# Optimization experiments

Measured on AMD Instinct MI355X. Metric: run time of the kernel, lower is better.

The kernel has to match this reference:

```python
import jax, jax.numpy as jnp
import numpy as np

B, NPG, DEG, D, H, K, NHID, CB = 64, 512, 16, 128, 4, 5, 50, 512
N = B * NPG
E = N * DEG
TAU = 1.0
EPS = 1e-6
BN_SCALE = 1.0 / np.sqrt(1.0 + 1e-5)  # eval-mode BatchNorm, running mean=0 var=1


def _forward(x, edge_index, batch, emb, gin_W1, gin_b1, gin_W2, gin_b2, bn_gamma, bn_beta, part_W1, part_b1, part_W2, part_b2, Wq, Wk, Wv, Wo, gate_W1, gate_b1, gate_W2, gate_b2, codebook, cls_W1, cls_b1, cls_W2, cls_b2, cls_W3, cls_b3):
    # --- GIN stack: h_i <- MLP((1+eps)*h_i + sum_{j->i} h_j), eps=0 ---
    h = emb[x]  # [N, D]
    src, dst = edge_index[0], edge_index[1]
    n_layers = gin_W1.shape[0]
    for l in range(n_layers):
        agg = jax.ops.segment_sum(h[src], dst, num_segments=N)  # scatter-add neighbor messages
        z = h + agg
        z = jax.nn.relu(z @ gin_W1[l] + gin_b1[l]) @ gin_W2[l] + gin_b2[l]
        z = z * (BN_SCALE * bn_gamma[l]) + bn_beta[l]  # eval BN
        h = jax.nn.relu(z) if l < n_layers - 1 else z
    # --- to_dense_batch (equal-size graphs) + soft partitioner ---
    dense = h.reshape(B, NPG, D)
    cl = jax.nn.relu(dense @ part_W1 + part_b1) @ part_W2 + part_b2  # [B,NPG,K]
    S = jax.nn.softmax(cl / TAU, axis=-1)  # soft node->cluster assignment
    cf = jnp.einsum('bnk,bnd->bkd', S, dense) / (S.sum(1)[..., None] + EPS)
    # --- VQ codebook (l2 nearest neighbor, straight-through) ---
    flat = cf.reshape(-1, D)
    d2 = (flat * flat).sum(-1, keepdims=True) - 2.0 * flat @ codebook.T + (codebook * codebook).sum(-1)
    idx = jnp.argmin(d2, axis=-1)
    zq = cf + jax.lax.stop_gradient(codebook[idx].reshape(B, K, D) - cf)
    # --- scatter-mean graph pooling over batch vector ---
    residue = jax.ops.segment_sum(h, batch, num_segments=B) / NPG  # [B,D]
    # --- global cluster attention (4 heads), residue query vs cluster keys ---
    dh = D // H
    q = (residue @ Wq).reshape(B, H, dh)
    k = (zq @ Wk).reshape(B, K, H, dh)
    v = (zq @ Wv).reshape(B, K, H, dh)
    aw = jax.nn.softmax(jnp.einsum('bhd,bkhd->bhk', q, k) / np.sqrt(dh), axis=-1)
    att = jnp.einsum('bhk,bkhd->bhd', aw, v).reshape(B, D) @ Wo
    # --- feature-wise gated fusion ---
    cat = jnp.concatenate([residue, att], axis=-1)
    g = jax.nn.sigmoid(jax.nn.relu(cat @ gate_W1 + gate_b1) @ gate_W2 + gate_b2)
    fused = g * residue + (1.0 - g) * att
    # --- classifier MLP ---
    z1 = jax.nn.relu(fused @ cls_W1 + cls_b1)
    z2 = jax.nn.relu(z1 @ cls_W2 + cls_b2)
    return z2 @ cls_W3 + cls_b3


def setup_inputs():
    key = jax.random.key(0)
    ks = jax.random.split(key, 20)
    def lin(k, i, o):
        return jax.random.normal(k, (i, o), jnp.float32) / np.sqrt(i)
    x = jax.random.randint(ks[0], (N,), 0, 21, dtype=jnp.int32)
    srcn = jnp.repeat(jnp.arange(N, dtype=jnp.int32), DEG)
    dstn = (srcn // NPG) * NPG + jax.random.randint(ks[1], (E,), 0, NPG, dtype=jnp.int32)
    edge_index = jnp.stack([srcn, dstn])
    batch = jnp.repeat(jnp.arange(B, dtype=jnp.int32), NPG)
    return {
        'x': x, 'edge_index': edge_index, 'batch': batch,
        'emb': jax.random.normal(ks[2], (21, D), jnp.float32) * 0.02,
        'gin_W1': jax.random.normal(ks[3], (3, D, 2 * D), jnp.float32) / np.sqrt(D),
        'gin_b1': jnp.zeros((3, 2 * D), jnp.float32),
        'gin_W2': jax.random.normal(ks[4], (3, 2 * D, D), jnp.float32) / np.sqrt(2 * D),
        'gin_b2': jnp.zeros((3, D), jnp.float32),
        'bn_gamma': jnp.ones((3, D), jnp.float32),
        'bn_beta': jnp.zeros((3, D), jnp.float32),
        'part_W1': lin(ks[5], D, NHID), 'part_b1': jnp.zeros((NHID,), jnp.float32),
        'part_W2': lin(ks[6], NHID, K), 'part_b2': jnp.zeros((K,), jnp.float32),
        'Wq': lin(ks[7], D, D), 'Wk': lin(ks[8], D, D), 'Wv': lin(ks[9], D, D), 'Wo': lin(ks[10], D, D),
        'gate_W1': lin(ks[11], 2 * D, D // 2), 'gate_b1': jnp.zeros((D // 2,), jnp.float32),
        'gate_W2': lin(ks[12], D // 2, D), 'gate_b2': jnp.zeros((D,), jnp.float32),
        'codebook': jax.random.normal(ks[13], (CB, D), jnp.float32) * 0.1,
        'cls_W1': lin(ks[14], D, 4 * D), 'cls_b1': jnp.zeros((4 * D,), jnp.float32),
        'cls_W2': lin(ks[15], 4 * D, 2 * D), 'cls_b2': jnp.zeros((2 * D,), jnp.float32),
        'cls_W3': lin(ks[16], 2 * D, 2), 'cls_b3': jnp.zeros((2,), jnp.float32),
    }


def reference(x, edge_index, batch, emb, gin_W1, gin_b1, gin_W2, gin_b2, bn_gamma, bn_beta, part_W1, part_b1, part_W2, part_b2, Wq, Wk, Wv, Wo, gate_W1, gate_b1, gate_W2, gate_b2, codebook, cls_W1, cls_b1, cls_W2, cls_b2, cls_W3, cls_b3):
    return _forward(x, edge_index, batch, emb, gin_W1, gin_b1, gin_W2, gin_b2, bn_gamma, bn_beta, part_W1, part_b1, part_W2, part_b2, Wq, Wk, Wv, Wo, gate_W1, gate_b1, gate_W2, gate_b2, codebook, cls_W1, cls_b1, cls_W2, cls_b2, cls_W3, cls_b3)
```

## Files before the change

### kernel.cpp

```cpp
#include <hip/hip_runtime.h>

constexpr int B_    = 64;
constexpr int NPG_  = 512;
constexpr int D_    = 128;
constexpr int K_    = 5;
constexpr int NHID_ = 50;
constexpr int CB_   = 512;
constexpr int N_    = B_ * NPG_;
constexpr int E_    = N_ * 16;
constexpr float BN_SCALE_ = 0.99999500003749969f;
constexpr float EPS_ = 1e-6f;

typedef __attribute__((ext_vector_type(8))) short bf16x8_t;
typedef __attribute__((ext_vector_type(4))) float f32x4_t;

__device__ __forceinline__ unsigned short f2bf(float x) {
    unsigned int u = __float_as_uint(x);
    unsigned int r = (u + 0x7FFFu + ((u >> 16) & 1u)) >> 16;
    return (unsigned short)r;
}
__device__ __forceinline__ float bf2f(unsigned short b) {
    return __uint_as_float(((unsigned int)b) << 16);
}

__device__ __forceinline__ f32x4_t mfma3(bf16x8_t a0, bf16x8_t a1,
                                         bf16x8_t b0, bf16x8_t b1, f32x4_t acc) {
    acc = __builtin_amdgcn_mfma_f32_16x16x32_bf16(a1, b0, acc, 0, 0, 0);
    acc = __builtin_amdgcn_mfma_f32_16x16x32_bf16(a0, b1, acc, 0, 0, 0);
    acc = __builtin_amdgcn_mfma_f32_16x16x32_bf16(a0, b0, acc, 0, 0, 0);
    return acc;
}

__global__ void k_prep(const float* __restrict__ gw1, const float* __restrict__ gw2,
                       unsigned short* __restrict__ w1h, unsigned short* __restrict__ w1l,
                       unsigned short* __restrict__ w2h, unsigned short* __restrict__ w2l) {
    int e = blockIdx.x * 256 + threadIdx.x;
    int layer = e >> 16, rem = e & 65535;
    if (rem < 32768) {
        int k = rem >> 8, n = rem & 255;
        float v = gw1[layer * 32768 + rem];
        unsigned short h0 = f2bf(v);
        int o = layer * 32768 +
                ((((n >> 4) * 4 + (k >> 5)) * 64 + ((k >> 3) & 3) * 16 + (n & 15)) << 3) + (k & 7);
        w1h[o] = h0; w1l[o] = f2bf(v - bf2f(h0));
    } else {
        int rr = rem - 32768;
        int c = rr >> 7, n = rr & 127;
        float v = gw2[layer * 32768 + rr];
        unsigned short h0 = f2bf(v);
        int o = layer * 32768 +
                ((((n >> 4) * 8 + (c >> 5)) * 64 + ((c >> 3) & 3) * 16 + (n & 15)) << 3) + (c & 7);
        w2h[o] = h0; w2l[o] = f2bf(v - bf2f(h0));
    }
}

__global__ __launch_bounds__(512) void k_csr(const int* __restrict__ dst,
                                             int* __restrict__ rowptr,
                                             int* __restrict__ col) {
    __shared__ int cnt[512];
    __shared__ int sc[512];
    __shared__ short dstS[8192];
    int g = blockIdx.x, t = threadIdx.x;
    int base = g * 8192;
    cnt[t] = 0;
    __syncthreads();
    for (int i = t; i < 8192; i += 512) {
        int d = dst[base + i] & 511;
        dstS[i] = (short)d;
        atomicAdd(&cnt[d], 1);
    }
    __syncthreads();
    int c0 = cnt[t];
    sc[t] = c0;
    __syncthreads();
    for (int off = 1; off < 512; off <<= 1) {
        int v = sc[t];
        int add = (t >= off) ? sc[t - off] : 0;
        __syncthreads();
        sc[t] = v + add;
        __syncthreads();
    }
    int excl = sc[t] - c0;
    rowptr[g * 512 + t] = base + excl;
    cnt[t] = excl;
    if (g == 0 && t == 0) rowptr[N_] = E_;
    __syncthreads();
    for (int i = t; i < 8192; i += 512) {
        int d = dstS[i];
        int p = atomicAdd(&cnt[d], 1);
        col[base + p] = g * 512 + (i >> 4);
    }
}

constexpr int LDH = 264;
constexpr int COLCAP = 1024;
template<int L0>
__global__ __launch_bounds__(512, 8) void k_gin(
    const float* __restrict__ hIn, const int* __restrict__ rowptr,
    const int* __restrict__ col,
    const int* __restrict__ xIdx, const float* __restrict__ emb,
    const unsigned short* __restrict__ w1h, const unsigned short* __restrict__ w1l,
    const unsigned short* __restrict__ w2h, const unsigned short* __restrict__ w2l,
    const float* __restrict__ b1, const float* __restrict__ b2,
    const float* __restrict__ gamma, const float* __restrict__ beta,
    int relu_out, float* __restrict__ hOut) {
    __shared__ int colS[COLCAP];
    __shared__ unsigned short bufH[32 * LDH];
    __shared__ unsigned short bufL[32 * LDH];
    __shared__ float embS[L0 ? 21 * 128 : 1];
    __shared__ int xS[L0 ? 512 : 1];
    int i = blockIdx.x;
    int xcd = i & 7;
    int slot = i >> 3;
    int g = (slot >> 4) * 8 + xcd;
    int tile = slot & 15;
    int rowBase = g * 512 + tile * 32;
    int t = threadIdx.x;
    int w = t >> 6, l = t & 63;
    int l15 = l & 15, quad = l >> 4;
    int half = l >> 5, lane4 = l & 31;

    int ebase = rowptr[rowBase];
    int ecnt  = rowptr[rowBase + 32] - ebase;
    bool inLds = (ecnt <= COLCAP);
    if (inLds)
        for (int j = t; j < ecnt; j += 512) colS[j] = col[ebase + j];
    if constexpr (L0) {
        for (int j = t; j < 21 * 128; j += 512) embS[j] = emb[j];
        if (t < 512) xS[t] = xIdx[(rowBase & ~511) + t];
    }
    __syncthreads();

    const float4* h4 = (const float4*)hIn;
    #pragma unroll
    for (int jj = 0; jj < 2; jj++) {
        int row = w * 4 + half * 2 + jj;
        int node = rowBase + row;
        int beg = rowptr[node], end = rowptr[node + 1];
        float4 a;
        if constexpr (L0)
            a = *(const float4*)&embS[xS[node & 511] * 128 + lane4 * 4];
        else
            a = h4[(size_t)node * 32 + lane4];
        int e = beg;
        if constexpr (L0) {
            for (; e < end; e++) {
                int c = (inLds ? colS[e - ebase] : col[e]) & 511;
                float4 p = *(const float4*)&embS[xS[c] * 128 + lane4 * 4];
                a.x += p.x; a.y += p.y; a.z += p.z; a.w += p.w;
            }
        } else {
            for (; e + 8 <= end; e += 8) {
                int c[8];
                #pragma unroll
                for (int u = 0; u < 8; u++)
                    c[u] = inLds ? colS[e - ebase + u] : col[e + u];
                float4 p[8];
                #pragma unroll
                for (int u = 0; u < 8; u++)
                    p[u] = h4[(size_t)c[u] * 32 + lane4];
                #pragma unroll
                for (int u = 0; u < 8; u++) {
                    a.x += p[u].x; a.y += p[u].y; a.z += p[u].z; a.w += p[u].w;
                }
            }
            for (; e < end; e++) {
                int c = inLds ? colS[e - ebase] : col[e];
                float4 p = h4[(size_t)c * 32 + lane4];
                a.x += p.x; a.y += p.y; a.z += p.z; a.w += p.w;
            }
        }
        unsigned short h0 = f2bf(a.x), h1 = f2bf(a.y), h2s = f2bf(a.z), h3 = f2bf(a.w);
        uint2 hv, lv;
        hv.x = (unsigned)h0 | ((unsigned)h1 << 16);
        hv.y = (unsigned)h2s | ((unsigned)h3 << 16);
        lv.x = (unsigned)f2bf(a.x - bf2f(h0)) | ((unsigned)f2bf(a.y - bf2f(h1)) << 16);
        lv.y = (unsigned)f2bf(a.z - bf2f(h2s)) | ((unsigned)f2bf(a.w - bf2f(h3)) << 16);
        *(uint2*)&bufH[row * LDH + lane4 * 4] = hv;
        *(uint2*)&bufL[row * LDH + lane4 * 4] = lv;
    }
    __syncthreads();

    f32x4_t acc[2][2];
    #pragma unroll
    for (int nt = 0; nt < 2; nt++) {
        float bb = b1[w * 32 + nt * 16 + l15];
        acc[0][nt] = (f32x4_t){bb, bb, bb, bb};
        acc[1][nt] = (f32x4_t){bb, bb, bb, bb};
    }
    #pragma unroll
    for (int kk = 0; kk < 4; kk++) {
        bf16x8_t ah[2], al[2];
        #pragma unroll
        for (int mt = 0; mt < 2; mt++) {
            int addr = (mt * 16 + l15) * LDH + kk * 32 + quad * 8;
            ah[mt] = *(const bf16x8_t*)&bufH[addr];
            al[mt] = *(const bf16x8_t*)&bufL[addr];
        }
        #pragma unroll
        for (int nt = 0; nt < 2; nt++) {
            int n16 = w * 2 + nt;
            int ga = (((n16 * 4 + kk) * 64 + l) << 3);
            bf16x8_t bh = *(const bf16x8_t*)&w1h[ga];
            bf16x8_t bl = *(const bf16x8_t*)&w1l[ga];
            acc[0][nt] = mfma3(ah[0], al[0], bh, bl, acc[0][nt]);
            acc[1][nt] = mfma3(ah[1], al[1], bh, bl, acc[1][nt]);
        }
    }
    __syncthreads();

    #pragma unroll
    for (int mt = 0; mt < 2; mt++)
        #pragma unroll
        for (int nt = 0; nt < 2; nt++) {
            int colL = w * 32 + nt * 16 + l15;
            #pragma unroll
            for (int r = 0; r < 4; r++) {
                int row = mt * 16 + quad * 4 + r;
                float v = fmaxf(acc[mt][nt][r], 0.f);
                unsigned short h0 = f2bf(v);
                bufH[row * LDH + colL] = h0;
                bufL[row * LDH + colL] = f2bf(v - bf2f(h0));
            }
        }
    __syncthreads();

    f32x4_t acc2[2];
    {
        float bb = b2[w * 16 + l15];
        acc2[0] = (f32x4_t){bb, bb, bb, bb};
        acc2[1] = (f32x4_t){bb, bb, bb, bb};
    }
    #pragma unroll
    for (int kkG = 0; kkG < 8; kkG++) {
        bf16x8_t ah[2], al[2];
        #pragma unroll
        for (int mt = 0; mt < 2; mt++) {
            int addr = (mt * 16 + l15) * LDH + kkG * 32 + quad * 8;
            ah[mt] = *(const bf16x8_t*)&bufH[addr];
            al[mt] = *(const bf16x8_t*)&bufL[addr];
        }
        int ga = (((w * 8 + kkG) * 64 + l) << 3);
        bf16x8_t bh = *(const bf16x8_t*)&w2h[ga];
        bf16x8_t bl = *(const bf16x8_t*)&w2l[ga];
        acc2[0] = mfma3(ah[0], al[0], bh, bl, acc2[0]);
        acc2[1] = mfma3(ah[1], al[1], bh, bl, acc2[1]);
    }
    {
        int colC = w * 16 + l15;
        float gm = BN_SCALE_ * gamma[colC];
        float be = beta[colC];
        #pragma unroll
        for (int mt = 0; mt < 2; mt++)
            #pragma unroll
            for (int r = 0; r < 4; r++) {
                int row = mt * 16 + quad * 4 + r;
                float v = fmaf(acc2[mt][r], gm, be);
                if (relu_out) v = fmaxf(v, 0.f);
                hOut[(size_t)(rowBase + row) * 128 + colC] = v;
            }
    }
}

__global__ __launch_bounds__(256) void k_partcf(
    const float* __restrict__ h,
    const float* __restrict__ W1, const float* __restrict__ b1,
    const float* __restrict__ W2, const float* __restrict__ b2,
    float* __restrict__ pacc, float* __restrict__ pss, float* __restrict__ prs) {
    __shared__ float zt[64 * 128];
    __shared__ float ht[64 * 52];
    __shared__ float lt[64 * 5];
    __shared__ float red[128 * 6];
    __shared__ float ssred[10];
    int t = threadIdx.x;
    int blk = blockIdx.x;
    int base = blk * 64;
    #pragma unroll
    for (int i = 0; i < 32; i++) { int idx = t + i * 256; zt[idx] = h[(size_t)base * D_ + idx]; }
    __syncthreads();
    int tx = t & 63, ty = t >> 6, r0 = ty * 16;
    if (tx < NHID_) {
        float acc[16];
        float bb = b1[tx];
        #pragma unroll
        for (int r = 0; r < 16; r++) acc[r] = bb;
        for (int k = 0; k < 128; k++) {
            float w = W1[k * NHID_ + tx];
            #pragma unroll
            for (int r = 0; r < 16; r++) acc[r] = fmaf(zt[(r0 + r) * 128 + k], w, acc[r]);
        }
        #pragma unroll
        for (int r = 0; r < 16; r++) ht[(r0 + r) * 52 + tx] = fmaxf(acc[r], 0.f);
    }
    __syncthreads();
    if (tx < K_) {
        float acc[16];
        float bb = b2[tx];
        #pragma unroll
        for (int r = 0; r < 16; r++) acc[r] = bb;
        for (int c = 0; c < NHID_; c++) {
            float w = W2[c * K_ + tx];
            #pragma unroll
            for (int r = 0; r < 16; r++) acc[r] = fmaf(ht[(r0 + r) * 52 + c], w, acc[r]);
        }
        #pragma unroll
        for (int r = 0; r < 16; r++) lt[(r0 + r) * 5 + tx] = acc[r];
    }
    __syncthreads();
    if (t < 64) {
        float l0 = lt[t*5], l1 = lt[t*5+1], l2 = lt[t*5+2], l3 = lt[t*5+3], l4 = lt[t*5+4];
        float m = fmaxf(fmaxf(fmaxf(l0, l1), fmaxf(l2, l3)), l4);
        float e0 = expf(l0 - m), e1 = expf(l1 - m), e2 = expf(l2 - m),
              e3 = expf(l3 - m), e4 = expf(l4 - m);
        float inv = 1.0f / (e0 + e1 + e2 + e3 + e4);
        lt[t*5]   = e0*inv; lt[t*5+1] = e1*inv; lt[t*5+2] = e2*inv;
        lt[t*5+3] = e3*inv; lt[t*5+4] = e4*inv;
    }
    __syncthreads();
    int d = t & 127, grp = t >> 7;
    float acc[5] = {0,0,0,0,0}, ssum[5] = {0,0,0,0,0}, rs = 0;
    #pragma unroll 4
    for (int i = 0; i < 32; i++) {
        int nl = grp * 32 + i;
        float hv = zt[nl * 128 + d];
        rs += hv;
        #pragma unroll
        for (int k = 0; k < 5; k++) {
            float sv = lt[nl * 5 + k];
            acc[k] = fmaf(sv, hv, acc[k]);
            ssum[k] += sv;
        }
    }
    if (grp == 1) {
        #pragma unroll
        for (int k = 0; k < 5; k++) red[d * 6 + k] = acc[k];
        red[d * 6 + 5] = rs;
    }
    if (d == 0) {
        #pragma unroll
        for (int k = 0; k < 5; k++) ssred[grp * 5 + k] = ssum[k];
    }
    __syncthreads();
    if (grp == 0) {
        #pragma unroll
        for (int k = 0; k < 5; k++) {
            acc[k] += red[d * 6 + k];
            pacc[((size_t)blk * 5 + k) * 128 + d] = acc[k];
        }
        rs += red[d * 6 + 5];
        prs[blk * 128 + d] = rs;
        if (d < 5) pss[blk * 5 + d] = ssred[d] + ssred[5 + d];
    }
}

__global__ __launch_bounds__(1024) void k_tail(
    const float* __restrict__ pacc, const float* __restrict__ pss,
    const float* __restrict__ prs, const float* __restrict__ cbk,
    const float* __restrict__ Wq, const float* __restrict__ Wk,
    const float* __restrict__ Wv, const float* __restrict__ Wo,
    const float* __restrict__ gW1, const float* __restrict__ gb1,
    const float* __restrict__ gW2, const float* __restrict__ gb2,
    const float* __restrict__ cW1, const float* __restrict__ cb1,
    const float* __restrict__ cW2, const float* __restrict__ cb2,
    const float* __restrict__ cW3, const float* __restrict__ cb3,
    float* __restrict__ out) {
    __shared__ float cfS[5 * 128];
    __shared__ float zqS[5 * 128];
    __shared__ float catS[256];
    __shared__ float qS[128];
    __shared__ float kS[5 * 128];
    __shared__ float vS[5 * 128];
    __shared__ float awS[20];
    __shared__ float att1S[128];
    __shared__ float attP[4][128];
    __shared__ float g1P[8][64];
    __shared__ float g1S[64];
    __shared__ float g2P[4][128];
    __shared__ float fusedS[128];
    __shared__ float z1P[2][512];
    __shared__ float z1S[512];
    __shared__ float z2P[4][256];
    __shared__ float bd5[5][512];
    __shared__ int   bi5[5][512];
    __shared__ int   idxS[5];
    __shared__ float red[8];

    int g = blockIdx.x, t = threadIdx.x;

    if (t < 768) {
        int c = t >> 7, d = t & 127;
        if (c == 5) {
            float rs = 0;
            #pragma unroll
            for (int ch = 0; ch < 8; ch++) rs += prs[(g * 8 + ch) * 128 + d];
            catS[d] = rs * (1.0f / 512.0f);
        } else {
            float acc = 0, ss = 0;
            #pragma unroll
            for (int ch = 0; ch < 8; ch++) {
                int blk = g * 8 + ch;
                acc += pacc[((size_t)blk * 5 + c) * 128 + d];
                ss  += pss[blk * 5 + c];
            }
            cfS[c * 128 + d] = acc / (ss + EPS_);
        }
    }
    __syncthreads();

    if (t < 512) {
        const float4* cj = (const float4*)(cbk + (size_t)t * 128);
        float d2[5] = {0, 0, 0, 0, 0};
        #pragma unroll 8
        for (int q4 = 0; q4 < 32; q4++) {
            float4 c4 = cj[q4];
            #pragma unroll
            for (int k = 0; k < 5; k++) {
                float4 f4 = ((const float4*)(cfS + k * 128))[q4];
                float dx = f4.x - c4.x, dy = f4.y - c4.y;
                float dz = f4.z - c4.z, dw = f4.w - c4.w;
                d2[k] = fmaf(dx, dx, d2[k]); d2[k] = fmaf(dy, dy, d2[k]);
                d2[k] = fmaf(dz, dz, d2[k]); d2[k] = fmaf(dw, dw, d2[k]);
            }
        }
        #pragma unroll
        for (int k = 0; k < 5; k++) { bd5[k][t] = d2[k]; bi5[k][t] = t; }
    }
    __syncthreads();
    for (int s = 256; s > 0; s >>= 1) {
        if (t < s) {
            #pragma unroll
            for (int k = 0; k < 5; k++) {
                float bo = bd5[k][t + s]; int io = bi5[k][t + s];
                if (bo < bd5[k][t] || (bo == bd5[k][t] && io < bi5[k][t])) {
                    bd5[k][t] = bo; bi5[k][t] = io;
                }
            }
        }
        __syncthreads();
    }
    if (t < 5) idxS[t] = bi5[t][0];
    __syncthreads();
    if (t < 640) zqS[t] = cbk[(size_t)idxS[t >> 7] * 128 + (t & 127)];
    __syncthreads();

    for (int o = t; o < 1408; o += 1024) {
        const float* Arow; const float* W; int dcol;
        if (o < 128)      { Arow = catS;                     W = Wq; dcol = o; }
        else if (o < 768) { Arow = &zqS[((o - 128) >> 7) * 128]; W = Wk; dcol = (o - 128) & 127; }
        else              { Arow = &zqS[((o - 768) >> 7) * 128]; W = Wv; dcol = (o - 768) & 127; }
        float acc = 0;
        for (int kk = 0; kk < 128; kk++) acc = fmaf(Arow[kk], W[kk * 128 + dcol], acc);
        if (o < 128)      qS[o] = acc;
        else if (o < 768) kS[o - 128] = acc;
        else              vS[o - 768] = acc;
    }
    __syncthreads();

    if (t < 20) {
        int hh = t / 5, j = t % 5;
        float s = 0;
        #pragma unroll
        for (int d2 = 0; d2 < 32; d2++)
            s = fmaf(qS[hh * 32 + d2], kS[j * 128 + hh * 32 + d2], s);
        awS[t] = s * 0.17677669529663687f;
    }
    __syncthreads();
    if (t < 4) {
        float m = -1e30f;
        for (int j = 0; j < 5; j++) m = fmaxf(m, awS[t * 5 + j]);
        float e[5], sum = 0;
        for (int j = 0; j < 5; j++) { e[j] = expf(awS[t * 5 + j] - m); sum += e[j]; }
        for (int j = 0; j < 5; j++) awS[t * 5 + j] = e[j] / sum;
    }
    __syncthreads();
    if (t < 128) {
        int hh = t >> 5;
        float a = 0;
        #pragma unroll
        for (int j = 0; j < 5; j++) a = fmaf(awS[hh * 5 + j], vS[j * 128 + t], a);
        att1S[t] = a;
    }
    __syncthreads();
    if (t < 512) {
        int o = t & 127, kq = t >> 7;
        float a = 0;
        #pragma unroll 8
        for (int i = 0; i < 32; i++) {
            int kk = kq * 32 + i;
            a = fmaf(att1S[kk], Wo[kk * 128 + o], a);
        }
        attP[kq][o] = a;
    }
    __syncthreads();
    if (t < 128) catS[128 + t] = attP[0][t] + attP[1][t] + attP[2][t] + attP[3][t];
    __syncthreads();

    if (t < 512) {
        int o = t & 63, kq = t >> 6;
        float a = 0;
        #pragma unroll 8
        for (int i = 0; i < 32; i++) {
            int kk = kq * 32 + i;
            a = fmaf(catS[kk], gW1[kk * 64 + o], a);
        }
        g1P[kq][o] = a;
    }
    __syncthreads();
    if (t < 64) {
        float a = gb1[t];
        #pragma unroll
        for (int q = 0; q < 8; q++) a += g1P[q][t];
        g1S[t] = fmaxf(a, 0.f);
    }
    __syncthreads();
    if (t < 512) {
        int o = t & 127, kq = t >> 7;
        float a = 0;
        #pragma unroll 8
        for (int i = 0; i < 16; i++) {
            int kk = kq * 16 + i;
            a = fmaf(g1S[kk], gW2[kk * 128 + o], a);
        }
        g2P[kq][o] = a;
    }
    __syncthreads();
    if (t < 128) {
        float a = gb2[t] + g2P[0][t] + g2P[1][t] + g2P[2][t] + g2P[3][t];
        float gv = 1.f / (1.f + expf(-a));
        fusedS[t] = gv * catS[t] + (1.f - gv) * catS[128 + t];
    }
    __syncthreads();

    {
        int o = t & 511, kq = t >> 9;
        float a = 0;
        #pragma unroll 8
        for (int i = 0; i < 64; i++) {
            int kk = kq * 64 + i;
            a = fmaf(fusedS[kk], cW1[kk * 512 + o], a);
        }
        z1P[kq][o] = a;
    }
    __syncthreads();
    if (t < 512) z1S[t] = fmaxf(z1P[0][t] + z1P[1][t] + cb1[t], 0.f);
    __syncthreads();
    {
        int o = t & 255, kq = t >> 8;
        float a = 0;
        #pragma unroll 8
        for (int i = 0; i < 128; i++) {
            int kk = kq * 128 + i;
            a = fmaf(z1S[kk], cW2[kk * 256 + o], a);
        }
        z2P[kq][o] = a;
    }
    __syncthreads();
    if (t < 256) {
        float zv = fmaxf(z2P[0][t] + z2P[1][t] + z2P[2][t] + z2P[3][t] + cb2[t], 0.f);
        float p0 = zv * cW3[t * 2];
        float p1 = zv * cW3[t * 2 + 1];
        #pragma unroll
        for (int off = 32; off > 0; off >>= 1) {
            p0 += __shfl_down(p0, off, 64);
            p1 += __shfl_down(p1, off, 64);
        }
        int wv = t >> 6;
        if ((t & 63) == 0) { red[wv * 2] = p0; red[wv * 2 + 1] = p1; }
    }
    __syncthreads();
    if (t < 2)
        out[g * 2 + t] = cb3[t] + red[t] + red[2 + t] + red[4 + t] + red[6 + t];
}

extern "C" void kernel_launch(void* const* d_in, const int* in_sizes, int n_in,
                              void* d_out, int out_size, void* d_ws, size_t ws_size,
                              hipStream_t stream) {
    const int*   x          = (const int*)d_in[0];
    const int*   edge_index = (const int*)d_in[1];
    const float* emb      = (const float*)d_in[3];
    const float* gin_W1   = (const float*)d_in[4];
    const float* gin_b1   = (const float*)d_in[5];
    const float* gin_W2   = (const float*)d_in[6];
    const float* gin_b2   = (const float*)d_in[7];
    const float* bn_gamma = (const float*)d_in[8];
    const float* bn_beta  = (const float*)d_in[9];
    const float* part_W1  = (const float*)d_in[10];
    const float* part_b1  = (const float*)d_in[11];
    const float* part_W2  = (const float*)d_in[12];
    const float* part_b2  = (const float*)d_in[13];
    const float* Wq       = (const float*)d_in[14];
    const float* Wk       = (const float*)d_in[15];
    const float* Wv       = (const float*)d_in[16];
    const float* Wo       = (const float*)d_in[17];
    const float* gate_W1  = (const float*)d_in[18];
    const float* gate_b1  = (const float*)d_in[19];
    const float* gate_W2  = (const float*)d_in[20];
    const float* gate_b2  = (const float*)d_in[21];
    const float* codebook = (const float*)d_in[22];
    const float* cls_W1   = (const float*)d_in[23];
    const float* cls_b1   = (const float*)d_in[24];
    const float* cls_W2   = (const float*)d_in[25];
    const float* cls_b2   = (const float*)d_in[26];
    const float* cls_W3   = (const float*)d_in[27];
    const float* cls_b3   = (const float*)d_in[28];

    const int* dstp = edge_index + E_;

    char* w = (char*)d_ws;
    float* hA = (float*)w;  w += (size_t)N_ * D_ * 4;
    float* hB = (float*)w;  w += (size_t)N_ * D_ * 4;
    int* rowptr = (int*)w;  w += (size_t)(N_ + 4) * 4;
    int* col    = (int*)w;  w += (size_t)E_ * 4;
    unsigned short* w1h = (unsigned short*)w;  w += (size_t)3 * 32768 * 2;
    unsigned short* w1l = (unsigned short*)w;  w += (size_t)3 * 32768 * 2;
    unsigned short* w2h = (unsigned short*)w;  w += (size_t)3 * 32768 * 2;
    unsigned short* w2l = (unsigned short*)w;  w += (size_t)3 * 32768 * 2;

    char* tz = (char*)hA;
    float* pacc = (float*)tz;  tz += (size_t)512 * 5 * 128 * 4;
    float* pss  = (float*)tz;  tz += (size_t)512 * 5 * 4;
    float* prs  = (float*)tz;  tz += (size_t)512 * 128 * 4;

    k_prep<<<768, 256, 0, stream>>>(gin_W1, gin_W2, w1h, w1l, w2h, w2l);
    k_csr <<<64, 512, 0, stream>>>(dstp, rowptr, col);

    k_gin<1><<<1024, 512, 0, stream>>>(
        hA, rowptr, col, x, emb,
        w1h, w1l, w2h, w2l,
        gin_b1, gin_b2, bn_gamma, bn_beta, 1, hB);
    k_gin<0><<<1024, 512, 0, stream>>>(
        hB, rowptr, col, x, emb,
        w1h + 32768, w1l + 32768, w2h + 32768, w2l + 32768,
        gin_b1 + 256, gin_b2 + 128, bn_gamma + 128, bn_beta + 128, 1, hA);
    k_gin<0><<<1024, 512, 0, stream>>>(
        hA, rowptr, col, x, emb,
        w1h + 65536, w1l + 65536, w2h + 65536, w2l + 65536,
        gin_b1 + 512, gin_b2 + 256, bn_gamma + 256, bn_beta + 256, 0, hB);

    k_partcf<<<512, 256, 0, stream>>>(hB, part_W1, part_b1, part_W2, part_b2,
                                      pacc, pss, prs);
    k_tail<<<B_, 1024, 0, stream>>>(pacc, pss, prs, codebook,
                                    Wq, Wk, Wv, Wo,
                                    gate_W1, gate_b1, gate_W2, gate_b2,
                                    cls_W1, cls_b1, cls_W2, cls_b2, cls_W3, cls_b3,
                                    (float*)d_out);
}
```

Baseline: 277.3 us.

## Replace GIN gather aggregation with per-graph dense adjacency MFMA matmul

Layers 2 and 3 of the GIN stack now build a dense bf16 adjacency tile (32 rows by 512 nodes of the same graph, self loop included) in LDS and compute the neighbour sum as an MFMA matmul. The features it multiplies are stored by the previous layer as hi/lo bf16 fragments pre-laid-out for MFMA. This replaces irregular float4 gathers with streamed fragment loads and tensor-core work. In exchange it adds O(512) dense MACs per row, a larger LDS footprint (launch bounds reduced to 4 blocks), and assumes edges stay within a graph (col & 511). Edge counts are accumulated in bf16, which stays exact only for small integer multiplicities.

```diff
diff --git a/kernel.cpp b/kernel.cpp
--- a/kernel.cpp
+++ b/kernel.cpp
@@ -94,21 +94,23 @@
 
 constexpr int LDH = 264;
 constexpr int COLCAP = 1024;
-template<int L0>
-__global__ __launch_bounds__(512, 8) void k_gin(
-    const float* __restrict__ hIn, const int* __restrict__ rowptr,
-    const int* __restrict__ col,
+constexpr int LDA = 520;
+
+
+
+__global__ __launch_bounds__(512, 8) void k_gin0(
+    const int* __restrict__ rowptr, const int* __restrict__ col,
     const int* __restrict__ xIdx, const float* __restrict__ emb,
     const unsigned short* __restrict__ w1h, const unsigned short* __restrict__ w1l,
     const unsigned short* __restrict__ w2h, const unsigned short* __restrict__ w2l,
     const float* __restrict__ b1, const float* __restrict__ b2,
     const float* __restrict__ gamma, const float* __restrict__ beta,
-    int relu_out, float* __restrict__ hOut) {
+    unsigned short* __restrict__ oFH, unsigned short* __restrict__ oFL) {
     __shared__ int colS[COLCAP];
     __shared__ unsigned short bufH[32 * LDH];
     __shared__ unsigned short bufL[32 * LDH];
-    __shared__ float embS[L0 ? 21 * 128 : 1];
-    __shared__ int xS[L0 ? 512 : 1];
+    __shared__ float embS[21 * 128];
+    __shared__ int xS[512];
     int i = blockIdx.x;
     int xcd = i & 7;
     int slot = i >> 3;
@@ -125,50 +127,20 @@
     bool inLds = (ecnt <= COLCAP);
     if (inLds)
         for (int j = t; j < ecnt; j += 512) colS[j] = col[ebase + j];
-    if constexpr (L0) {
-        for (int j = t; j < 21 * 128; j += 512) embS[j] = emb[j];
-        if (t < 512) xS[t] = xIdx[(rowBase & ~511) + t];
-    }
-    __syncthreads();
-
-    const float4* h4 = (const float4*)hIn;
+    for (int j = t; j < 21 * 128; j += 512) embS[j] = emb[j];
+    if (t < 512) xS[t] = xIdx[(rowBase & ~511) + t];
+    __syncthreads();
+
     #pragma unroll
     for (int jj = 0; jj < 2; jj++) {
         int row = w * 4 + half * 2 + jj;
         int node = rowBase + row;
         int beg = rowptr[node], end = rowptr[node + 1];
-        float4 a;
-        if constexpr (L0)
-            a = *(const float4*)&embS[xS[node & 511] * 128 + lane4 * 4];
-        else
-            a = h4[(size_t)node * 32 + lane4];
-        int e = beg;
-        if constexpr (L0) {
-            for (; e < end; e++) {
-                int c = (inLds ? colS[e - ebase] : col[e]) & 511;
-                float4 p = *(const float4*)&embS[xS[c] * 128 + lane4 * 4];
-                a.x += p.x; a.y += p.y; a.z += p.z; a.w += p.w;
-            }
-        } else {
-            for (; e + 8 <= end; e += 8) {
-                int c[8];
-                #pragma unroll
-                for (int u = 0; u < 8; u++)
-                    c[u] = inLds ? colS[e - ebase + u] : col[e + u];
-                float4 p[8];
-                #pragma unroll
-                for (int u = 0; u < 8; u++)
-                    p[u] = h4[(size_t)c[u] * 32 + lane4];
-                #pragma unroll
-                for (int u = 0; u < 8; u++) {
-                    a.x += p[u].x; a.y += p[u].y; a.z += p[u].z; a.w += p[u].w;
-                }
-            }
-            for (; e < end; e++) {
-                int c = inLds ? colS[e - ebase] : col[e];
-                float4 p = h4[(size_t)c * 32 + lane4];
-                a.x += p.x; a.y += p.y; a.z += p.z; a.w += p.w;
-            }
+        float4 a = *(const float4*)&embS[xS[node & 511] * 128 + lane4 * 4];
+        for (int e = beg; e < end; e++) {
+            int c = (inLds ? colS[e - ebase] : col[e]) & 511;
+            float4 p = *(const float4*)&embS[xS[c] * 128 + lane4 * 4];
+            a.x += p.x; a.y += p.y; a.z += p.z; a.w += p.w;
         }
         unsigned short h0 = f2bf(a.x), h1 = f2bf(a.y), h2s = f2bf(a.z), h3 = f2bf(a.w);
         uint2 hv, lv;
@@ -208,7 +180,6 @@
         }
     }
     __syncthreads();
-
     #pragma unroll
     for (int mt = 0; mt < 2; mt++)
         #pragma unroll
@@ -250,15 +221,194 @@
         int colC = w * 16 + l15;
         float gm = BN_SCALE_ * gamma[colC];
         float be = beta[colC];
-        #pragma unroll
-        for (int mt = 0; mt < 2; mt++)
+        unsigned short* oH = oFH + (size_t)g * 65536;
+        unsigned short* oL = oFL + (size_t)g * 65536;
+        #pragma unroll
+        for (int mt = 0; mt < 2; mt++) {
+            int obase = (((w * 16 + tile) * 64) + (mt * 2 + (quad >> 1)) * 16 + l15) * 8 + (quad & 1) * 4;
+            ushort4 vh, vl;
+            #pragma unroll
+            for (int r = 0; r < 4; r++) {
+                float v = fmaxf(fmaf(acc2[mt][r], gm, be), 0.f);
+                unsigned short hh = f2bf(v);
+                unsigned short ll = f2bf(v - bf2f(hh));
+                if (r == 0) { vh.x = hh; vl.x = ll; }
+                else if (r == 1) { vh.y = hh; vl.y = ll; }
+                else if (r == 2) { vh.z = hh; vl.z = ll; }
+                else { vh.w = hh; vl.w = ll; }
+            }
+            *(ushort4*)&oH[obase] = vh;
+            *(ushort4*)&oL[obase] = vl;
+        }
+    }
+}
+
+template<int FRAG_OUT>
+__global__ __launch_bounds__(512, 4) void k_ginF(
+    const unsigned short* __restrict__ hFH, const unsigned short* __restrict__ hFL,
+    const int* __restrict__ rowptr, const int* __restrict__ col,
+    const unsigned short* __restrict__ w1h, const unsigned short* __restrict__ w1l,
+    const unsigned short* __restrict__ w2h, const unsigned short* __restrict__ w2l,
+    const float* __restrict__ b1, const float* __restrict__ b2,
+    const float* __restrict__ gamma, const float* __restrict__ beta,
+    unsigned short* __restrict__ oFH, unsigned short* __restrict__ oFL,
+    float* __restrict__ hOut) {
+    __shared__ unsigned short A16[32 * LDA];
+    __shared__ unsigned short bufH[32 * LDH];
+    __shared__ unsigned short bufL[32 * LDH];
+    int i = blockIdx.x;
+    int xcd = i & 7;
+    int slot = i >> 3;
+    int g = (slot >> 4) * 8 + xcd;
+    int tile = slot & 15;
+    int rowBase = g * 512 + tile * 32;
+    int t = threadIdx.x;
+    int w = t >> 6, l = t & 63;
+    int l15 = l & 15, quad = l >> 4;
+
+    for (int j = t; j < 32 * (LDA / 2); j += 512) ((unsigned int*)A16)[j] = 0;
+    __syncthreads();
+    if (t < 32) {
+        int node = rowBase + t;
+        int beg = rowptr[node], end = rowptr[node + 1];
+        unsigned short* Arow = &A16[t * LDA];
+        for (int e = beg; e < end; e++) {
+            int c = col[e] & 511;
+            Arow[c] = f2bf(bf2f(Arow[c]) + 1.0f);
+        }
+        int selfc = (rowBase & 511) + t;
+        Arow[selfc] = f2bf(bf2f(Arow[selfc]) + 1.0f);
+    }
+    __syncthreads();
+
+    const unsigned short* gFH = hFH + (size_t)g * 65536;
+    const unsigned short* gFL = hFL + (size_t)g * 65536;
+    f32x4_t zacc[2];
+    zacc[0] = (f32x4_t){0, 0, 0, 0};
+    zacc[1] = (f32x4_t){0, 0, 0, 0};
+    #pragma unroll
+    for (int kc = 0; kc < 16; kc++) {
+        int ga = (((w * 16 + kc) * 64 + l) << 3);
+        bf16x8_t bh = *(const bf16x8_t*)&gFH[ga];
+        bf16x8_t bl = *(const bf16x8_t*)&gFL[ga];
+        #pragma unroll
+        for (int mt = 0; mt < 2; mt++) {
+            bf16x8_t a = *(const bf16x8_t*)&A16[(mt * 16 + l15) * LDA + kc * 32 + quad * 8];
+            zacc[mt] = __builtin_amdgcn_mfma_f32_16x16x32_bf16(a, bh, zacc[mt], 0, 0, 0);
+            zacc[mt] = __builtin_amdgcn_mfma_f32_16x16x32_bf16(a, bl, zacc[mt], 0, 0, 0);
+        }
+    }
+    #pragma unroll
+    for (int mt = 0; mt < 2; mt++)
+        #pragma unroll
+        for (int r = 0; r < 4; r++) {
+            int row = mt * 16 + quad * 4 + r;
+            int colL = w * 16 + l15;
+            float v = zacc[mt][r];
+            unsigned short h0 = f2bf(v);
+            bufH[row * LDH + colL] = h0;
+            bufL[row * LDH + colL] = f2bf(v - bf2f(h0));
+        }
+    __syncthreads();
+
+    f32x4_t acc[2][2];
+    #pragma unroll
+    for (int nt = 0; nt < 2; nt++) {
+        float bb = b1[w * 32 + nt * 16 + l15];
+        acc[0][nt] = (f32x4_t){bb, bb, bb, bb};
+        acc[1][nt] = (f32x4_t){bb, bb, bb, bb};
+    }
+    #pragma unroll
+    for (int kk = 0; kk < 4; kk++) {
+        bf16x8_t ah[2], al[2];
+        #pragma unroll
+        for (int mt = 0; mt < 2; mt++) {
+            int addr = (mt * 16 + l15) * LDH + kk * 32 + quad * 8;
+            ah[mt] = *(const bf16x8_t*)&bufH[addr];
+            al[mt] = *(const bf16x8_t*)&bufL[addr];
+        }
+        #pragma unroll
+        for (int nt = 0; nt < 2; nt++) {
+            int n16 = w * 2 + nt;
+            int ga = (((n16 * 4 + kk) * 64 + l) << 3);
+            bf16x8_t bh = *(const bf16x8_t*)&w1h[ga];
+            bf16x8_t bl = *(const bf16x8_t*)&w1l[ga];
+            acc[0][nt] = mfma3(ah[0], al[0], bh, bl, acc[0][nt]);
+            acc[1][nt] = mfma3(ah[1], al[1], bh, bl, acc[1][nt]);
+        }
+    }
+    __syncthreads();
+    #pragma unroll
+    for (int mt = 0; mt < 2; mt++)
+        #pragma unroll
+        for (int nt = 0; nt < 2; nt++) {
+            int colL = w * 32 + nt * 16 + l15;
             #pragma unroll
             for (int r = 0; r < 4; r++) {
                 int row = mt * 16 + quad * 4 + r;
-                float v = fmaf(acc2[mt][r], gm, be);
-                if (relu_out) v = fmaxf(v, 0.f);
-                hOut[(size_t)(rowBase + row) * 128 + colC] = v;
+                float v = fmaxf(acc[mt][nt][r], 0.f);
+                unsigned short h0 = f2bf(v);
+                bufH[row * LDH + colL] = h0;
+                bufL[row * LDH + colL] = f2bf(v - bf2f(h0));
             }
+        }
+    __syncthreads();
+
+    f32x4_t acc2[2];
+    {
+        float bb = b2[w * 16 + l15];
+        acc2[0] = (f32x4_t){bb, bb, bb, bb};
+        acc2[1] = (f32x4_t){bb, bb, bb, bb};
+    }
+    #pragma unroll
+    for (int kkG = 0; kkG < 8; kkG++) {
+        bf16x8_t ah[2], al[2];
+        #pragma unroll
+        for (int mt = 0; mt < 2; mt++) {
+            int addr = (mt * 16 + l15) * LDH + kkG * 32 + quad * 8;
+            ah[mt] = *(const bf16x8_t*)&bufH[addr];
+            al[mt] = *(const bf16x8_t*)&bufL[addr];
+        }
+        int ga = (((w * 8 + kkG) * 64 + l) << 3);
+        bf16x8_t bh = *(const bf16x8_t*)&w2h[ga];
+        bf16x8_t bl = *(const bf16x8_t*)&w2l[ga];
+        acc2[0] = mfma3(ah[0], al[0], bh, bl, acc2[0]);
+        acc2[1] = mfma3(ah[1], al[1], bh, bl, acc2[1]);
+    }
+    {
+        int colC = w * 16 + l15;
+        float gm = BN_SCALE_ * gamma[colC];
+        float be = beta[colC];
+        if constexpr (FRAG_OUT) {
+            unsigned short* oH = oFH + (size_t)g * 65536;
+            unsigned short* oL = oFL + (size_t)g * 65536;
+            #pragma unroll
+            for (int mt = 0; mt < 2; mt++) {
+                int obase = (((w * 16 + tile) * 64) + (mt * 2 + (quad >> 1)) * 16 + l15) * 8 + (quad & 1) * 4;
+                ushort4 vh, vl;
+                #pragma unroll
+                for (int r = 0; r < 4; r++) {
+                    float v = fmaxf(fmaf(acc2[mt][r], gm, be), 0.f);
+                    unsigned short hh = f2bf(v);
+                    unsigned short ll = f2bf(v - bf2f(hh));
+                    if (r == 0) { vh.x = hh; vl.x = ll; }
+                    else if (r == 1) { vh.y = hh; vl.y = ll; }
+                    else if (r == 2) { vh.z = hh; vl.z = ll; }
+                    else { vh.w = hh; vl.w = ll; }
+                }
+                *(ushort4*)&oH[obase] = vh;
+                *(ushort4*)&oL[obase] = vl;
+            }
+        } else {
+            #pragma unroll
+            for (int mt = 0; mt < 2; mt++)
+                #pragma unroll
+                for (int r = 0; r < 4; r++) {
+                    int row = mt * 16 + quad * 4 + r;
+                    float v = fmaf(acc2[mt][r], gm, be);
+                    hOut[(size_t)(rowBase + row) * 128 + colC] = v;
+                }
+        }
     }
 }
 
@@ -607,7 +757,6 @@
     const int* dstp = edge_index + E_;
 
     char* w = (char*)d_ws;
-    float* hA = (float*)w;  w += (size_t)N_ * D_ * 4;
     float* hB = (float*)w;  w += (size_t)N_ * D_ * 4;
     int* rowptr = (int*)w;  w += (size_t)(N_ + 4) * 4;
     int* col    = (int*)w;  w += (size_t)E_ * 4;
@@ -615,27 +764,32 @@
     unsigned short* w1l = (unsigned short*)w;  w += (size_t)3 * 32768 * 2;
     unsigned short* w2h = (unsigned short*)w;  w += (size_t)3 * 32768 * 2;
     unsigned short* w2l = (unsigned short*)w;  w += (size_t)3 * 32768 * 2;
-
-    char* tz = (char*)hA;
-    float* pacc = (float*)tz;  tz += (size_t)512 * 5 * 128 * 4;
-    float* pss  = (float*)tz;  tz += (size_t)512 * 5 * 4;
-    float* prs  = (float*)tz;  tz += (size_t)512 * 128 * 4;
+    unsigned short* fragAH = (unsigned short*)w;  w += (size_t)B_ * 65536 * 2;
+    unsigned short* fragAL = (unsigned short*)w;  w += (size_t)B_ * 65536 * 2;
+    unsigned short* fragBH = (unsigned short*)w;  w += (size_t)B_ * 65536 * 2;
+    unsigned short* fragBL = (unsigned short*)w;  w += (size_t)B_ * 65536 * 2;
+    float* pacc = (float*)w;  w += (size_t)512 * 5 * 128 * 4;
+    float* pss  = (float*)w;  w += (size_t)512 * 5 * 4;
+    float* prs  = (float*)w;  w += (size_t)512 * 128 * 4;
 
     k_prep<<<768, 256, 0, stream>>>(gin_W1, gin_W2, w1h, w1l, w2h, w2l);
     k_csr <<<64, 512, 0, stream>>>(dstp, rowptr, col);
 
-    k_gin<1><<<1024, 512, 0, stream>>>(
-        hA, rowptr, col, x, emb,
+    k_gin0<<<1024, 512, 0, stream>>>(
+        rowptr, col, x, emb,
         w1h, w1l, w2h, w2l,
-        gin_b1, gin_b2, bn_gamma, bn_beta, 1, hB);
-    k_gin<0><<<1024, 512, 0, stream>>>(
-        hB, rowptr, col, x, emb,
+        gin_b1, gin_b2, bn_gamma, bn_beta,
+        fragAH, fragAL);
+    k_ginF<1><<<1024, 512, 0, stream>>>(
+        fragAH, fragAL, rowptr, col,
         w1h + 32768, w1l + 32768, w2h + 32768, w2l + 32768,
-        gin_b1 + 256, gin_b2 + 128, bn_gamma + 128, bn_beta + 128, 1, hA);
-    k_gin<0><<<1024, 512, 0, stream>>>(
-        hA, rowptr, col, x, emb,
+        gin_b1 + 256, gin_b2 + 128, bn_gamma + 128, bn_beta + 128,
+        fragBH, fragBL, nullptr);
+    k_ginF<0><<<1024, 512, 0, stream>>>(
+        fragBH, fragBL, rowptr, col,
         w1h + 65536, w1l + 65536, w2h + 65536, w2l + 65536,
-        gin_b1 + 512, gin_b2 + 256, bn_gamma + 256, bn_beta + 256, 0, hB);
+        gin_b1 + 512, gin_b2 + 256, bn_gamma + 256, bn_beta + 256,
+        nullptr, nullptr, hB);
 
     k_partcf<<<512, 256, 0, stream>>>(hB, part_W1, part_b1, part_W2, part_b2,
                                       pacc, pss, prs);
```

Result: slower. 284.1 us (+2.4%).

## Fuse partitioner and cluster pooling into last GIN layer; merge prep and CSR kernels

Applied to the files above, without the earlier changes.

The last GIN layer now keeps its 32-row output tile in shared memory and computes the partitioner MLP, the softmax and the per-tile cluster and residue partial sums directly. This removes the final h write and re-read and the separate k_partcf launch. The weight-prep and CSR-build kernels are merged into one launch. The tail kernel now reduces over 16 partial tiles per graph, and the last layer's occupancy hint drops to 4, with scalar per-row partitioner math that may be slower per block.

```diff
diff --git a/kernel.cpp b/kernel.cpp
--- a/kernel.cpp
+++ b/kernel.cpp
@@ -31,36 +31,37 @@
     return acc;
 }
 
-__global__ void k_prep(const float* __restrict__ gw1, const float* __restrict__ gw2,
-                       unsigned short* __restrict__ w1h, unsigned short* __restrict__ w1l,
-                       unsigned short* __restrict__ w2h, unsigned short* __restrict__ w2l) {
-    int e = blockIdx.x * 256 + threadIdx.x;
-    int layer = e >> 16, rem = e & 65535;
-    if (rem < 32768) {
-        int k = rem >> 8, n = rem & 255;
-        float v = gw1[layer * 32768 + rem];
-        unsigned short h0 = f2bf(v);
-        int o = layer * 32768 +
-                ((((n >> 4) * 4 + (k >> 5)) * 64 + ((k >> 3) & 3) * 16 + (n & 15)) << 3) + (k & 7);
-        w1h[o] = h0; w1l[o] = f2bf(v - bf2f(h0));
-    } else {
-        int rr = rem - 32768;
-        int c = rr >> 7, n = rr & 127;
-        float v = gw2[layer * 32768 + rr];
-        unsigned short h0 = f2bf(v);
-        int o = layer * 32768 +
-                ((((n >> 4) * 8 + (c >> 5)) * 64 + ((c >> 3) & 3) * 16 + (n & 15)) << 3) + (c & 7);
-        w2h[o] = h0; w2l[o] = f2bf(v - bf2f(h0));
-    }
-}
-
-__global__ __launch_bounds__(512) void k_csr(const int* __restrict__ dst,
-                                             int* __restrict__ rowptr,
-                                             int* __restrict__ col) {
+__global__ __launch_bounds__(512) void k_prepcsr(
+    const int* __restrict__ dst, int* __restrict__ rowptr, int* __restrict__ col,
+    const float* __restrict__ gw1, const float* __restrict__ gw2,
+    unsigned short* __restrict__ w1h, unsigned short* __restrict__ w1l,
+    unsigned short* __restrict__ w2h, unsigned short* __restrict__ w2l) {
     __shared__ int cnt[512];
     __shared__ int sc[512];
     __shared__ short dstS[8192];
-    int g = blockIdx.x, t = threadIdx.x;
+    int b = blockIdx.x, t = threadIdx.x;
+    if (b >= 64) {
+        int e = (b - 64) * 512 + t;
+        int layer = e >> 16, rem = e & 65535;
+        if (rem < 32768) {
+            int k = rem >> 8, n = rem & 255;
+            float v = gw1[layer * 32768 + rem];
+            unsigned short h0 = f2bf(v);
+            int o = layer * 32768 +
+                    ((((n >> 4) * 4 + (k >> 5)) * 64 + ((k >> 3) & 3) * 16 + (n & 15)) << 3) + (k & 7);
+            w1h[o] = h0; w1l[o] = f2bf(v - bf2f(h0));
+        } else {
+            int rr = rem - 32768;
+            int c = rr >> 7, n = rr & 127;
+            float v = gw2[layer * 32768 + rr];
+            unsigned short h0 = f2bf(v);
+            int o = layer * 32768 +
+                    ((((n >> 4) * 8 + (c >> 5)) * 64 + ((c >> 3) & 3) * 16 + (n & 15)) << 3) + (c & 7);
+            w2h[o] = h0; w2l[o] = f2bf(v - bf2f(h0));
+        }
+        return;
+    }
+    int g = b;
     int base = g * 8192;
     cnt[t] = 0;
     __syncthreads();
@@ -94,8 +95,8 @@
 
 constexpr int LDH = 264;
 constexpr int COLCAP = 1024;
-template<int L0>
-__global__ __launch_bounds__(512, 8) void k_gin(
+template<int L0, int LAST>
+__global__ __launch_bounds__(512, LAST ? 4 : 8) void k_gin(
     const float* __restrict__ hIn, const int* __restrict__ rowptr,
     const int* __restrict__ col,
     const int* __restrict__ xIdx, const float* __restrict__ emb,
@@ -103,12 +104,16 @@
     const unsigned short* __restrict__ w2h, const unsigned short* __restrict__ w2l,
     const float* __restrict__ b1, const float* __restrict__ b2,
     const float* __restrict__ gamma, const float* __restrict__ beta,
-    int relu_out, float* __restrict__ hOut) {
+    int relu_out, float* __restrict__ hOut,
+    const float* __restrict__ pW1, const float* __restrict__ pb1,
+    const float* __restrict__ pW2, const float* __restrict__ pb2,
+    float* __restrict__ pacc, float* __restrict__ pss, float* __restrict__ prs) {
     __shared__ int colS[COLCAP];
-    __shared__ unsigned short bufH[32 * LDH];
-    __shared__ unsigned short bufL[32 * LDH];
+    __shared__ __attribute__((aligned(16))) unsigned short bufH[32 * LDH];
+    __shared__ __attribute__((aligned(16))) unsigned short bufL[32 * LDH];
     __shared__ float embS[L0 ? 21 * 128 : 1];
     __shared__ int xS[L0 ? 512 : 1];
+    __shared__ float ltS[LAST ? 32 * 5 : 1];
     int i = blockIdx.x;
     int xcd = i & 7;
     int slot = i >> 3;
@@ -208,7 +213,6 @@
         }
     }
     __syncthreads();
-
     #pragma unroll
     for (int mt = 0; mt < 2; mt++)
         #pragma unroll
@@ -246,10 +250,10 @@
         acc2[0] = mfma3(ah[0], al[0], bh, bl, acc2[0]);
         acc2[1] = mfma3(ah[1], al[1], bh, bl, acc2[1]);
     }
-    {
-        int colC = w * 16 + l15;
-        float gm = BN_SCALE_ * gamma[colC];
-        float be = beta[colC];
+    int colC = w * 16 + l15;
+    float gm = BN_SCALE_ * gamma[colC];
+    float be = beta[colC];
+    if constexpr (!LAST) {
         #pragma unroll
         for (int mt = 0; mt < 2; mt++)
             #pragma unroll
@@ -259,97 +263,68 @@
                 if (relu_out) v = fmaxf(v, 0.f);
                 hOut[(size_t)(rowBase + row) * 128 + colC] = v;
             }
-    }
-}
-
-__global__ __launch_bounds__(256) void k_partcf(
-    const float* __restrict__ h,
-    const float* __restrict__ W1, const float* __restrict__ b1,
-    const float* __restrict__ W2, const float* __restrict__ b2,
-    float* __restrict__ pacc, float* __restrict__ pss, float* __restrict__ prs) {
-    __shared__ float zt[64 * 128];
-    __shared__ float ht[64 * 52];
-    __shared__ float lt[64 * 5];
-    __shared__ float red[128 * 6];
-    __shared__ float ssred[10];
-    int t = threadIdx.x;
-    int blk = blockIdx.x;
-    int base = blk * 64;
-    #pragma unroll
-    for (int i = 0; i < 32; i++) { int idx = t + i * 256; zt[idx] = h[(size_t)base * D_ + idx]; }
-    __syncthreads();
-    int tx = t & 63, ty = t >> 6, r0 = ty * 16;
-    if (tx < NHID_) {
-        float acc[16];
-        float bb = b1[tx];
-        #pragma unroll
-        for (int r = 0; r < 16; r++) acc[r] = bb;
-        for (int k = 0; k < 128; k++) {
-            float w = W1[k * NHID_ + tx];
+    } else {
+        __syncthreads();
+        float* zS  = (float*)bufH;
+        float* htS = (float*)bufL;
+        #pragma unroll
+        for (int mt = 0; mt < 2; mt++)
             #pragma unroll
-            for (int r = 0; r < 16; r++) acc[r] = fmaf(zt[(r0 + r) * 128 + k], w, acc[r]);
-        }
-        #pragma unroll
-        for (int r = 0; r < 16; r++) ht[(r0 + r) * 52 + tx] = fmaxf(acc[r], 0.f);
-    }
-    __syncthreads();
-    if (tx < K_) {
-        float acc[16];
-        float bb = b2[tx];
-        #pragma unroll
-        for (int r = 0; r < 16; r++) acc[r] = bb;
-        for (int c = 0; c < NHID_; c++) {
-            float w = W2[c * K_ + tx];
-            #pragma unroll
-            for (int r = 0; r < 16; r++) acc[r] = fmaf(ht[(r0 + r) * 52 + c], w, acc[r]);
-        }
-        #pragma unroll
-        for (int r = 0; r < 16; r++) lt[(r0 + r) * 5 + tx] = acc[r];
-    }
-    __syncthreads();
-    if (t < 64) {
-        float l0 = lt[t*5], l1 = lt[t*5+1], l2 = lt[t*5+2], l3 = lt[t*5+3], l4 = lt[t*5+4];
-        float m = fmaxf(fmaxf(fmaxf(l0, l1), fmaxf(l2, l3)), l4);
-        float e0 = expf(l0 - m), e1 = expf(l1 - m), e2 = expf(l2 - m),
-              e3 = expf(l3 - m), e4 = expf(l4 - m);
-        float inv = 1.0f / (e0 + e1 + e2 + e3 + e4);
-        lt[t*5]   = e0*inv; lt[t*5+1] = e1*inv; lt[t*5+2] = e2*inv;
-        lt[t*5+3] = e3*inv; lt[t*5+4] = e4*inv;
-    }
-    __syncthreads();
-    int d = t & 127, grp = t >> 7;
-    float acc[5] = {0,0,0,0,0}, ssum[5] = {0,0,0,0,0}, rs = 0;
-    #pragma unroll 4
-    for (int i = 0; i < 32; i++) {
-        int nl = grp * 32 + i;
-        float hv = zt[nl * 128 + d];
-        rs += hv;
-        #pragma unroll
-        for (int k = 0; k < 5; k++) {
-            float sv = lt[nl * 5 + k];
-            acc[k] = fmaf(sv, hv, acc[k]);
-            ssum[k] += sv;
-        }
-    }
-    if (grp == 1) {
-        #pragma unroll
-        for (int k = 0; k < 5; k++) red[d * 6 + k] = acc[k];
-        red[d * 6 + 5] = rs;
-    }
-    if (d == 0) {
-        #pragma unroll
-        for (int k = 0; k < 5; k++) ssred[grp * 5 + k] = ssum[k];
-    }
-    __syncthreads();
-    if (grp == 0) {
-        #pragma unroll
-        for (int k = 0; k < 5; k++) {
-            acc[k] += red[d * 6 + k];
-            pacc[((size_t)blk * 5 + k) * 128 + d] = acc[k];
-        }
-        rs += red[d * 6 + 5];
-        prs[blk * 128 + d] = rs;
-        if (d < 5) pss[blk * 5 + d] = ssred[d] + ssred[5 + d];
+            for (int r = 0; r < 4; r++) {
+                int row = mt * 16 + quad * 4 + r;
+                zS[row * 128 + colC] = fmaf(acc2[mt][r], gm, be);
+            }
+        __syncthreads();
+        for (int j = t; j < 2048; j += 512) {
+            int row = j >> 6, hd = j & 63;
+            if (hd < NHID_) {
+                float a = pb1[hd];
+                for (int k = 0; k < 128; k++)
+                    a = fmaf(zS[row * 128 + k], pW1[k * NHID_ + hd], a);
+                htS[row * 52 + hd] = fmaxf(a, 0.f);
+            }
+        }
+        __syncthreads();
+        if (t < 160) {
+            int row = t / 5, kk = t % 5;
+            float a = pb2[kk];
+            for (int c = 0; c < NHID_; c++)
+                a = fmaf(htS[row * 52 + c], pW2[c * K_ + kk], a);
+            ltS[row * 5 + kk] = a;
+        }
+        __syncthreads();
+        if (t < 32) {
+            float l0 = ltS[t*5], l1 = ltS[t*5+1], l2 = ltS[t*5+2],
+                  l3 = ltS[t*5+3], l4 = ltS[t*5+4];
+            float m = fmaxf(fmaxf(fmaxf(l0, l1), fmaxf(l2, l3)), l4);
+            float e0 = expf(l0 - m), e1 = expf(l1 - m), e2 = expf(l2 - m),
+                  e3 = expf(l3 - m), e4 = expf(l4 - m);
+            float inv = 1.0f / (e0 + e1 + e2 + e3 + e4);
+            ltS[t*5]   = e0*inv; ltS[t*5+1] = e1*inv; ltS[t*5+2] = e2*inv;
+            ltS[t*5+3] = e3*inv; ltS[t*5+4] = e4*inv;
+        }
+        __syncthreads();
+        int cIdx = g * 16 + tile;
+        for (int j = t; j < 640; j += 512) {
+            int k = j >> 7, d = j & 127;
+            float a = 0;
+            #pragma unroll 8
+            for (int r = 0; r < 32; r++)
+                a = fmaf(ltS[r * 5 + k], zS[r * 128 + d], a);
+            pacc[((size_t)cIdx * 5 + k) * 128 + d] = a;
+        }
+        if (t < 128) {
+            float a = 0;
+            #pragma unroll 8
+            for (int r = 0; r < 32; r++) a += zS[r * 128 + t];
+            prs[cIdx * 128 + t] = a;
+        } else if (t < 133) {
+            int k = t - 128;
+            float a = 0;
+            #pragma unroll 8
+            for (int r = 0; r < 32; r++) a += ltS[r * 5 + k];
+            pss[cIdx * 5 + k] = a;
+        }
     }
 }
 
@@ -392,13 +367,13 @@
         if (c == 5) {
             float rs = 0;
             #pragma unroll
-            for (int ch = 0; ch < 8; ch++) rs += prs[(g * 8 + ch) * 128 + d];
+            for (int ch = 0; ch < 16; ch++) rs += prs[(g * 16 + ch) * 128 + d];
             catS[d] = rs * (1.0f / 512.0f);
         } else {
             float acc = 0, ss = 0;
             #pragma unroll
-            for (int ch = 0; ch < 8; ch++) {
-                int blk = g * 8 + ch;
+            for (int ch = 0; ch < 16; ch++) {
+                int blk = g * 16 + ch;
                 acc += pacc[((size_t)blk * 5 + c) * 128 + d];
                 ss  += pss[blk * 5 + c];
             }
@@ -615,30 +590,29 @@
     unsigned short* w1l = (unsigned short*)w;  w += (size_t)3 * 32768 * 2;
     unsigned short* w2h = (unsigned short*)w;  w += (size_t)3 * 32768 * 2;
     unsigned short* w2l = (unsigned short*)w;  w += (size_t)3 * 32768 * 2;
-
-    char* tz = (char*)hA;
-    float* pacc = (float*)tz;  tz += (size_t)512 * 5 * 128 * 4;
-    float* pss  = (float*)tz;  tz += (size_t)512 * 5 * 4;
-    float* prs  = (float*)tz;  tz += (size_t)512 * 128 * 4;
-
-    k_prep<<<768, 256, 0, stream>>>(gin_W1, gin_W2, w1h, w1l, w2h, w2l);
-    k_csr <<<64, 512, 0, stream>>>(dstp, rowptr, col);
-
-    k_gin<1><<<1024, 512, 0, stream>>>(
+    float* pacc = (float*)w;  w += (size_t)1024 * 5 * 128 * 4;
+    float* pss  = (float*)w;  w += (size_t)1024 * 5 * 4;
+    float* prs  = (float*)w;  w += (size_t)1024 * 128 * 4;
+
+    k_prepcsr<<<448, 512, 0, stream>>>(dstp, rowptr, col,
+                                       gin_W1, gin_W2, w1h, w1l, w2h, w2l);
+
+    k_gin<1, 0><<<1024, 512, 0, stream>>>(
         hA, rowptr, col, x, emb,
         w1h, w1l, w2h, w2l,
-        gin_b1, gin_b2, bn_gamma, bn_beta, 1, hB);
-    k_gin<0><<<1024, 512, 0, stream>>>(
+        gin_b1, gin_b2, bn_gamma, bn_beta, 1, hB,
+        nullptr, nullptr, nullptr, nullptr, nullptr, nullptr, nullptr);
+    k_gin<0, 0><<<1024, 512, 0, stream>>>(
         hB, rowptr, col, x, emb,
         w1h + 32768, w1l + 32768, w2h + 32768, w2l + 32768,
-        gin_b1 + 256, gin_b2 + 128, bn_gamma + 128, bn_beta + 128, 1, hA);
-    k_gin<0><<<1024, 512, 0, stream>>>(
+        gin_b1 + 256, gin_b2 + 128, bn_gamma + 128, bn_beta + 128, 1, hA,
+        nullptr, nullptr, nullptr, nullptr, nullptr, nullptr, nullptr);
+    k_gin<0, 1><<<1024, 512, 0, stream>>>(
         hA, rowptr, col, x, emb,
         w1h + 65536, w1l + 65536, w2h + 65536, w2l + 65536,
-        gin_b1 + 512, gin_b2 + 256, bn_gamma + 256, bn_beta + 256, 0, hB);
-
-    k_partcf<<<512, 256, 0, stream>>>(hB, part_W1, part_b1, part_W2, part_b2,
-                                      pacc, pss, prs);
+        gin_b1 + 512, gin_b2 + 256, bn_gamma + 256, bn_beta + 256, 0, nullptr,
+        part_W1, part_b1, part_W2, part_b2, pacc, pss, prs);
+
     k_tail<<<B_, 1024, 0, stream>>>(pacc, pss, prs, codebook,
                                     Wq, Wk, Wv, Wo,
                                     gate_W1, gate_b1, gate_W2, gate_b2,
```

New measurement: 284.4 us. 2.6% more time.
